# Performance work log

Hardware: AMD Instinct MI355X
Metric: run time of the kernel (lower is better)

Reference implementation:

```python
import jax, jax.numpy as jnp
import numpy as np

DIM = 128
P = (2, 2, 2)
D_STATE = 8
D_CONV = 4
EXPAND = 2
D_INNER = EXPAND * DIM
DT_RANK = (DIM + 15) // 16  # ceil(d_model/16) = 8
EPS = 1e-5


def setup_inputs() -> dict:
    key = jax.random.key(0)
    ks = jax.random.split(key, 8)
    B, C, Z, H, W = 2, DIM, 40, 40, 40
    s = lambda k, shape, scale: jax.random.normal(k, shape, jnp.float32) * scale
    return {
        "x": jax.random.normal(ks[0], (B, C, Z, H, W), jnp.float32),
        "norm_g": jnp.ones((C,), jnp.float32),
        "norm_b": jnp.zeros((C,), jnp.float32),
        "in_proj_w": s(ks[1], (2 * D_INNER, C), 0.02),
        "conv_w": s(ks[2], (D_INNER, D_CONV), 0.1),
        "conv_b": jnp.zeros((D_INNER,), jnp.float32),
        "x_proj_w": s(ks[3], (DT_RANK + 2 * D_STATE, D_INNER), 0.02),
        "dt_proj_w": s(ks[4], (D_INNER, DT_RANK), 0.1),
        # softplus^-1(0.01): small positive init for delta, as in mamba_ssm
        "dt_bias": jnp.log(jnp.expm1(jnp.full((D_INNER,), 0.01, jnp.float32))),
        # S4D-real init: A_log = log([1..d_state]) per channel
        "A_log": jnp.log(jnp.tile(jnp.arange(1, D_STATE + 1, dtype=jnp.float32), (D_INNER, 1))),
        "D_vec": jnp.ones((D_INNER,), jnp.float32),
        "out_proj_w": s(ks[5], (DIM, D_INNER), 0.02),
    }


def _mamba(xn, in_proj_w, conv_w, conv_b, x_proj_w, dt_proj_w, dt_bias, A_log, D_vec, out_proj_w):
    # xn: (NB, L, C)
    NB, L, _ = xn.shape
    xz = jnp.einsum('blc,ec->ble', xn, in_proj_w)          # (NB, L, 2*d_inner)
    xp, z = jnp.split(xz, 2, axis=-1)
    # causal depthwise conv1d, kernel D_CONV, truncated to L
    xpad = jnp.pad(xp, ((0, 0), (D_CONV - 1, 0), (0, 0)))
    conv = conv_b
    for k in range(D_CONV):
        conv = conv + xpad[:, k:k + L, :] * conv_w[:, k]
    u = jax.nn.silu(conv)                                  # (NB, L, d_inner)
    xdbl = jnp.einsum('bld,ed->ble', u, x_proj_w)
    dt, Bm, Cm = jnp.split(xdbl, [DT_RANK, DT_RANK + D_STATE], axis=-1)
    delta = jax.nn.softplus(jnp.einsum('blr,dr->bld', dt, dt_proj_w) + dt_bias)
    A = -jnp.exp(A_log)                                    # (d_inner, d_state)

    def step(h, inp):
        d_t, B_t, C_t, u_t = inp  # (NB,d_inner),(NB,d_state),(NB,d_state),(NB,d_inner)
        h = jnp.exp(d_t[:, :, None] * A) * h + (d_t * u_t)[:, :, None] * B_t[:, None, :]
        return h, jnp.einsum('bds,bs->bd', h, C_t)

    h0 = jnp.zeros((NB, D_INNER, D_STATE), xn.dtype)
    xs = (jnp.swapaxes(delta, 0, 1), jnp.swapaxes(Bm, 0, 1),
          jnp.swapaxes(Cm, 0, 1), jnp.swapaxes(u, 0, 1))
    _, ys = jax.lax.scan(step, h0, xs)                     # ys: (L, NB, d_inner)
    y = jnp.swapaxes(ys, 0, 1) + u * D_vec
    y = y * jax.nn.silu(z)
    return jnp.einsum('bld,cd->blc', y, out_proj_w)        # (NB, L, C)


def reference(x, norm_g, norm_b, in_proj_w, conv_w, conv_b, x_proj_w, dt_proj_w,
              dt_bias, A_log, D_vec, out_proj_w):
    B, C, Z, H, W = x.shape
    p1, p2, p3 = P
    NZ, NH, NW = Z // p1, H // p2, W // p3
    NB, L = B * p1 * p2 * p3, NZ * NH * NW
    # patch reshuffle: (B,C,Z,H,W) -> (B*p1*p2*p3, C, NZ, NH, NW)
    xd = x.reshape(B, C, NZ, p1, NH, p2, NW, p3).transpose(0, 3, 5, 7, 1, 2, 4, 6)
    xf = jnp.swapaxes(xd.reshape(NB, C, L), 1, 2)          # (NB, L, C)
    # LayerNorm over channel dim
    mu = xf.mean(-1, keepdims=True)
    var = xf.var(-1, keepdims=True)
    xn = (xf - mu) * jax.lax.rsqrt(var + EPS) * norm_g + norm_b
    yo = _mamba(xn, in_proj_w, conv_w, conv_b, x_proj_w, dt_proj_w, dt_bias,
                A_log, D_vec, out_proj_w)                  # (NB, L, C)
    # undo reshuffle
    xo = jnp.swapaxes(yo, 1, 2).reshape(B, p1, p2, p3, C, NZ, NH, NW)
    xo = xo.transpose(0, 4, 5, 1, 6, 2, 7, 3).reshape(B, C, Z, H, W)
    return xo + x
```

## Files before the change

kernel.cpp:

```cpp
#include <hip/hip_runtime.h>

#define NBATCH 16
#define LSEQ   8000
#define MROWS  128000
#define CDIM   128
#define DI     256
#define DS     8
#define DTR    8
#define NXP    24
#define NC     250
#define CL     32

#define OFF_PB    0ull
#define OFF_XN    1024000ull
#define OFF_STA   1024000ull
#define OFF_XP    33792000ull
#define OFF_XDBL  33792000ull
#define OFF_STH   46080000ull
#define OFF_ZS    99328000ull
#define OFF_U     164864000ull
#define WS_NEEDED 230400000ull

#define P_G    0
#define P_B    128
#define P_IPW  256
#define P_CW   65792
#define P_CB   66816
#define P_XPW  67072
#define P_DTW  73216
#define P_DTB  75264
#define P_ALOG 75520
#define P_DVEC 77568
#define P_OPW  77824
#define P_TOT  110592

typedef __attribute__((ext_vector_type(8))) short bf16x8;
typedef __attribute__((ext_vector_type(4))) float f32x4;
typedef __attribute__((ext_vector_type(2))) float f32x2;

__device__ __forceinline__ float bf2f(unsigned short a) {
    union { unsigned int u; float f; } v; v.u = ((unsigned int)a) << 16; return v.f;
}
__device__ __forceinline__ unsigned short f2bf(float f) {
    union { float f; unsigned int u; } v; v.f = f;
    unsigned int r = v.u + 0x7FFFu + ((v.u >> 16) & 1u);
    return (unsigned short)(r >> 16);
}
__device__ __forceinline__ unsigned short f2bf_cvt(float f) {
    unsigned int r;
    asm("v_cvt_pk_bf16_f32 %0, %1, %2" : "=v"(r) : "v"(f), "v"(0.f));
    return (unsigned short)r;
}
__device__ __forceinline__ bool bfmode(const void* g) {
    return ((const unsigned int*)g)[0] == 0x3F803F80u;
}
__device__ __forceinline__ float rd(const void* p, size_t i, bool bf) {
    return bf ? bf2f(((const unsigned short*)p)[i]) : ((const float*)p)[i];
}
__device__ __forceinline__ f32x2 pk_fma(f32x2 a, f32x2 b, f32x2 c) {
    f32x2 d;
    asm("v_pk_fma_f32 %0, %1, %2, %3" : "=v"(d) : "v"(a), "v"(b), "v"(c));
    return d;
}
__device__ __forceinline__ f32x2 pk_mul(f32x2 a, f32x2 b) {
    f32x2 d;
    asm("v_pk_mul_f32 %0, %1, %2" : "=v"(d) : "v"(a), "v"(b));
    return d;
}
__device__ __forceinline__ int m_of(int b, int sp) {
    int z = sp / 1600;
    int rem = sp - z * 1600;
    int h = rem / 40;
    int w = rem - h * 40;
    int nb = b * 8 + (z & 1) * 4 + (h & 1) * 2 + (w & 1);
    int l = (z >> 1) * 400 + (h >> 1) * 20 + (w >> 1);
    return nb * LSEQ + l;
}

__global__ __launch_bounds__(256) void param_convert(const void* g, const void* b, const void* ipw,
                                                     const void* cw, const void* cb, const void* xpw,
                                                     const void* dtw, const void* dtb, const void* alog,
                                                     const void* dvec, const void* opw,
                                                     unsigned short* __restrict__ pb)
{
    int gid = blockIdx.x * 256 + threadIdx.x;
    if (gid >= P_TOT) return;
    bool bf = bfmode(g);
    const void* src; int off;
    if      (gid < P_B)    { src = g;    off = P_G; }
    else if (gid < P_IPW)  { src = b;    off = P_B; }
    else if (gid < P_CW)   { src = ipw;  off = P_IPW; }
    else if (gid < P_CB)   { src = cw;   off = P_CW; }
    else if (gid < P_XPW)  { src = cb;   off = P_CB; }
    else if (gid < P_DTW)  { src = xpw;  off = P_XPW; }
    else if (gid < P_DTB)  { src = dtw;  off = P_DTW; }
    else if (gid < P_ALOG) { src = dtb;  off = P_DTB; }
    else if (gid < P_DVEC) { src = alog; off = P_ALOG; }
    else if (gid < P_OPW)  { src = dvec; off = P_DVEC; }
    else                   { src = opw;  off = P_OPW; }
    pb[gid] = f2bf(rd(src, gid - off, bf));
}

__global__ __launch_bounds__(256) void lnorm_kernel(const void* __restrict__ x,
                                                    const unsigned short* __restrict__ pb,
                                                    unsigned short* __restrict__ xn)
{
    __shared__ float tile[128][65];
    __shared__ float psum[4][64], psqs[4][64];
    __shared__ float smu[64], srs[64];
    int b  = blockIdx.y;
    int sp0 = blockIdx.x * 64;
    int t = threadIdx.x;

    int spi = t & 63, cpart = t >> 6;
    const float* xf = (const float*)x;
#pragma unroll
    for (int pass = 0; pass < 32; ++pass) {
        int c = pass * 4 + cpart;
        tile[c][spi] = xf[((size_t)b * CDIM + c) * 64000 + sp0 + spi];
    }
    __syncthreads();

    {
        float s = 0.f, ss = 0.f;
        int c0 = cpart * 32;
#pragma unroll
        for (int cc = 0; cc < 32; ++cc) {
            float v = tile[c0 + cc][spi];
            s += v; ss += v * v;
        }
        psum[cpart][spi] = s; psqs[cpart][spi] = ss;
    }
    __syncthreads();
    if (cpart == 0) {
        float s  = psum[0][spi] + psum[1][spi] + psum[2][spi] + psum[3][spi];
        float ss = psqs[0][spi] + psqs[1][spi] + psqs[2][spi] + psqs[3][spi];
        float m = s * (1.f / CDIM);
        float var = ss * (1.f / CDIM) - m * m;
        smu[spi] = m;
        srs[spi] = rsqrtf(var + 1e-5f);
    }
    __syncthreads();

    int c = t & 127, half = t >> 7;
    float gc = bf2f(pb[P_G + c]), bc = bf2f(pb[P_B + c]);
#pragma unroll
    for (int pass = 0; pass < 32; ++pass) {
        int j = pass * 2 + half;
        int m = m_of(b, sp0 + j);
        float v = (tile[c][j] - smu[j]) * srs[j] * gc + bc;
        xn[(size_t)m * CDIM + c] = f2bf(v);
    }
}

__global__ __launch_bounds__(256) void gemm_bt_kernel(const unsigned short* __restrict__ A,
                                                      const unsigned short* __restrict__ W,
                                                      void* __restrict__ D,
                                                      int K, int Nact, int ldd, int act)
{
    __shared__ unsigned short As[128 * 32];
    __shared__ unsigned short Ws[128 * 32];
    int tid = threadIdx.x;
    int m0 = blockIdx.x * 128;
    int n0 = blockIdx.y * 128;
    int wave = tid >> 6, lane = tid & 63;
    int wm = (wave & 1) * 64, wn = (wave >> 1) * 64;
    int lrow = lane & 15, lk = (lane >> 4) * 8;
    int quad = lane >> 4;

    f32x4 acc[4][4];
#pragma unroll
    for (int i = 0; i < 4; i++)
#pragma unroll
        for (int j = 0; j < 4; j++) acc[i][j] = (f32x4){0.f, 0.f, 0.f, 0.f};

    int rowA0 = tid >> 2, kcA0 = (tid & 3) << 3;
    int rowA1 = (tid + 256) >> 2, kcA1 = (tid & 3) << 3;

    for (int kt = 0; kt < K; kt += 32) {
        *(uint4*)&As[rowA0 * 32 + kcA0] = *(const uint4*)&A[(size_t)(m0 + rowA0) * K + kt + kcA0];
        *(uint4*)&As[rowA1 * 32 + kcA1] = *(const uint4*)&A[(size_t)(m0 + rowA1) * K + kt + kcA1];
        uint4 z4 = {0u, 0u, 0u, 0u};
        uint4 w0 = (n0 + rowA0 < Nact) ? *(const uint4*)&W[(size_t)(n0 + rowA0) * K + kt + kcA0] : z4;
        uint4 w1 = (n0 + rowA1 < Nact) ? *(const uint4*)&W[(size_t)(n0 + rowA1) * K + kt + kcA1] : z4;
        *(uint4*)&Ws[rowA0 * 32 + kcA0] = w0;
        *(uint4*)&Ws[rowA1 * 32 + kcA1] = w1;
        __syncthreads();

        bf16x8 af[4], bfr[4];
#pragma unroll
        for (int i = 0; i < 4; i++) af[i]  = *(const bf16x8*)&As[(wm + i * 16 + lrow) * 32 + lk];
#pragma unroll
        for (int j = 0; j < 4; j++) bfr[j] = *(const bf16x8*)&Ws[(wn + j * 16 + lrow) * 32 + lk];
#pragma unroll
        for (int i = 0; i < 4; i++)
#pragma unroll
            for (int j = 0; j < 4; j++)
                acc[i][j] = __builtin_amdgcn_mfma_f32_16x16x32_bf16(af[i], bfr[j], acc[i][j], 0, 0, 0);
        __syncthreads();
    }

#pragma unroll
    for (int i = 0; i < 4; i++)
#pragma unroll
        for (int j = 0; j < 4; j++) {
            int n = n0 + wn + j * 16 + lrow;
            if (n < Nact) {
#pragma unroll
                for (int r = 0; r < 4; r++) {
                    int m = m0 + wm + i * 16 + quad * 4 + r;
                    float v = acc[i][j][r];
                    if (act == 1) v = v / (1.f + __expf(-v));
                    ((unsigned short*)D)[(size_t)m * ldd + n] = f2bf(v);
                }
            }
        }
}

__global__ __launch_bounds__(256) void gemm_conv_kernel(const unsigned short* __restrict__ A,
                                                        const unsigned short* __restrict__ W,
                                                        const unsigned short* __restrict__ cw,
                                                        const unsigned short* __restrict__ cb,
                                                        unsigned short* __restrict__ u)
{
    __shared__ unsigned short As[128 * 32];
    __shared__ unsigned short Ws[128 * 32];
    __shared__ unsigned short Dt[128 * 132];

    int tid = threadIdx.x;
    int tile = blockIdx.x & 63;
    int nb = blockIdx.x >> 6;
    int n0 = blockIdx.y * 128;
    int m0 = nb * 8000 + tile * 125;
    int mA = m0 - 3;
    int wave = tid >> 6, lane = tid & 63;
    int wm = (wave & 1) * 64, wn = (wave >> 1) * 64;
    int lrow = lane & 15, lk = (lane >> 4) * 8;
    int quad = lane >> 4;

    f32x4 acc[4][4];
#pragma unroll
    for (int i = 0; i < 4; i++)
#pragma unroll
        for (int j = 0; j < 4; j++) acc[i][j] = (f32x4){0.f, 0.f, 0.f, 0.f};

    int rowA0 = tid >> 2, kcA0 = (tid & 3) << 3;
    int rowA1 = (tid + 256) >> 2;

    for (int kt = 0; kt < CDIM; kt += 32) {
        uint4 z4 = {0u, 0u, 0u, 0u};
        uint4 a0 = (tile == 0 && rowA0 < 3) ? z4
                 : *(const uint4*)&A[(size_t)(mA + rowA0) * CDIM + kt + kcA0];
        uint4 a1 = *(const uint4*)&A[(size_t)(mA + rowA1) * CDIM + kt + kcA0];
        *(uint4*)&As[rowA0 * 32 + kcA0] = a0;
        *(uint4*)&As[rowA1 * 32 + kcA0] = a1;
        *(uint4*)&Ws[rowA0 * 32 + kcA0] = *(const uint4*)&W[(size_t)(n0 + rowA0) * CDIM + kt + kcA0];
        *(uint4*)&Ws[rowA1 * 32 + kcA0] = *(const uint4*)&W[(size_t)(n0 + rowA1) * CDIM + kt + kcA0];
        __syncthreads();

        bf16x8 af[4], bfr[4];
#pragma unroll
        for (int i = 0; i < 4; i++) af[i]  = *(const bf16x8*)&As[(wm + i * 16 + lrow) * 32 + lk];
#pragma unroll
        for (int j = 0; j < 4; j++) bfr[j] = *(const bf16x8*)&Ws[(wn + j * 16 + lrow) * 32 + lk];
#pragma unroll
        for (int i = 0; i < 4; i++)
#pragma unroll
            for (int j = 0; j < 4; j++)
                acc[i][j] = __builtin_amdgcn_mfma_f32_16x16x32_bf16(af[i], bfr[j], acc[i][j], 0, 0, 0);
        __syncthreads();
    }

#pragma unroll
    for (int i = 0; i < 4; i++)
#pragma unroll
        for (int j = 0; j < 4; j++) {
            int nl = wn + j * 16 + lrow;
            int tr = wm + i * 16 + quad * 4;
            unsigned int c01, c23;
            asm("v_cvt_pk_bf16_f32 %0, %1, %2" : "=v"(c01) : "v"(acc[i][j][0]), "v"(acc[i][j][1]));
            asm("v_cvt_pk_bf16_f32 %0, %1, %2" : "=v"(c23) : "v"(acc[i][j][2]), "v"(acc[i][j][3]));
            *(unsigned int*)&Dt[nl * 132 + tr]     = c01;
            *(unsigned int*)&Dt[nl * 132 + tr + 2] = c23;
        }
    __syncthreads();

    {
        int nl = tid & 127, half = tid >> 7;
        int dch = n0 + nl;
        float cw0 = bf2f(cw[dch * 4 + 0]), cw1 = bf2f(cw[dch * 4 + 1]);
        float cw2 = bf2f(cw[dch * 4 + 2]), cw3 = bf2f(cw[dch * 4 + 3]);
        float cbv = bf2f(cb[dch]);
        int tr0 = half ? 66 : 3;
        int nsteps = half ? 62 : 63;
        const unsigned short* col = &Dt[nl * 132];
        float x0 = bf2f(col[tr0 - 3]), x1 = bf2f(col[tr0 - 2]), x2 = bf2f(col[tr0 - 1]);
        unsigned short* uout = &u[(size_t)(m0 + tr0 - 3) * DI + dch];
#pragma unroll 1
        for (int k = 0; k < nsteps; ++k) {
            float x3 = bf2f(col[tr0 + k]);
            float a = cbv + cw0 * x0 + cw1 * x1 + cw2 * x2 + cw3 * x3;
            float uv = a * __builtin_amdgcn_rcpf(1.f + __expf(-a));
            *uout = f2bf_cvt(uv);
            uout += DI;
            x0 = x1; x1 = x2; x2 = x3;
        }
    }
}


#define BODY1(UR, RO) do {                                                       \
    union { f32x4 q; f32x2 h[2]; } qa, qb, qc, qd;                               \
    qa.q = *(const f32x4*)(rfp + (RO));                                          \
    qb.q = *(const f32x4*)(rfp + (RO) + 4);                                      \
    qc.q = *(const f32x4*)(rfp + (RO) + 8);                                      \
    qd.q = *(const f32x4*)(rfp + (RO) + 12);                                     \
    f32x2 din2 = pk_fma(qa.h[0], Wq[0], bias2);                                  \
    din2 = pk_fma(qa.h[1], Wq[1], din2);                                         \
    din2 = pk_fma(qb.h[0], Wq[2], din2);                                         \
    din2 = pk_fma(qb.h[1], Wq[3], din2);                                         \
    float din = din2.x + din2.y;                                                 \
    float e = __expf(din);                                                       \
    float w = 1.f + e;                                                           \
    float p1 = __builtin_amdgcn_rcpf(w);                                         \
    float delta = (din > 15.f) ? din : __logf(w);                                \
    float du = delta * bf2f(UR);                                                 \
    float p2 = p1 * p1;                                                          \
    f32x2 q1; q1.x = p1; q1.y = p2;                                              \
    f32x2 pp2; pp2.x = p2; pp2.y = p2;                                           \
    f32x2 q2 = pk_mul(q1, pp2);                                                  \
    f32x2 pp4; pp4.x = q2.y; pp4.y = q2.y;                                       \
    f32x2 q3 = pk_mul(q1, pp4);                                                  \
    f32x2 q4 = pk_mul(q2, pp4);                                                  \
    f32x2 du2; du2.x = du; du2.y = du;                                           \
    h2[0] = pk_fma(du2, qc.h[0], pk_mul(q1, h2[0]));                             \
    h2[1] = pk_fma(du2, qc.h[1], pk_mul(q2, h2[1]));                             \
    h2[2] = pk_fma(du2, qd.h[0], pk_mul(q3, h2[2]));                             \
    h2[3] = pk_fma(du2, qd.h[1], pk_mul(q4, h2[3]));                             \
    P *= p1;                                                                     \
} while (0)

__global__ __launch_bounds__(256) void gemm_xdbl_scan1(const unsigned short* __restrict__ u,
                                                       const unsigned short* __restrict__ W,
                                                       const unsigned short* __restrict__ dtw,
                                                       const unsigned short* __restrict__ dtb,
                                                       const unsigned short* __restrict__ alog,
                                                       float* __restrict__ xdbl,
                                                       float* __restrict__ stA,
                                                       float* __restrict__ stH)
{
    __shared__ unsigned short As[64 * 32];
    __shared__ unsigned short Ws[32 * 32];
    __shared__ float Dxs[64 * NXP];
    int tid = threadIdx.x;
    int m0 = blockIdx.x * 64;
    int wave = tid >> 6, lane = tid & 63;
    int wm = (wave & 1) * 32, wn = (wave >> 1) * 16;
    int lrow = lane & 15, lk = (lane >> 4) * 8;
    int quad = lane >> 4;

    f32x4 acc[2];
    acc[0] = (f32x4){0.f, 0.f, 0.f, 0.f};
    acc[1] = (f32x4){0.f, 0.f, 0.f, 0.f};

    int rowA = tid >> 2, kcA = (tid & 3) << 3;

    for (int kt = 0; kt < DI; kt += 32) {
        *(uint4*)&As[rowA * 32 + kcA] = *(const uint4*)&u[(size_t)(m0 + rowA) * DI + kt + kcA];
        if (tid < 128) {
            uint4 z4 = {0u, 0u, 0u, 0u};
            int rw = tid >> 2;
            uint4 w0 = (rw < NXP) ? *(const uint4*)&W[(size_t)rw * DI + kt + kcA] : z4;
            *(uint4*)&Ws[rw * 32 + kcA] = w0;
        }
        __syncthreads();

        bf16x8 af0 = *(const bf16x8*)&As[(wm + lrow) * 32 + lk];
        bf16x8 af1 = *(const bf16x8*)&As[(wm + 16 + lrow) * 32 + lk];
        bf16x8 bfr = *(const bf16x8*)&Ws[(wn + lrow) * 32 + lk];
        acc[0] = __builtin_amdgcn_mfma_f32_16x16x32_bf16(af0, bfr, acc[0], 0, 0, 0);
        acc[1] = __builtin_amdgcn_mfma_f32_16x16x32_bf16(af1, bfr, acc[1], 0, 0, 0);
        __syncthreads();
    }

    {
        int n = wn + lrow;
        if (n < NXP) {
#pragma unroll
            for (int i = 0; i < 2; i++)
#pragma unroll
                for (int r = 0; r < 4; r++) {
                    int ml = wm + i * 16 + quad * 4 + r;
                    float v = acc[i][r];
                    xdbl[(size_t)(m0 + ml) * NXP + n] = v;
                    Dxs[ml * NXP + n] = v;
                }
        }
    }
    __syncthreads();

    int d = tid;
    f32x2 Wq[4];
#pragma unroll
    for (int r = 0; r < 4; r++) {
        Wq[r].x = bf2f(dtw[d * DTR + 2 * r]);
        Wq[r].y = bf2f(dtw[d * DTR + 2 * r + 1]);
    }
    float Av[DS];
#pragma unroll
    for (int s = 0; s < DS; s++) Av[s] = -__expf(bf2f(alog[d * DS + s]));
    float A1 = Av[0];
    bool fast = (A1 == -1.0f);
#pragma unroll
    for (int s = 1; s < DS; s++)
        fast = fast && (fabsf(Av[s] - (float)(s + 1) * A1) <= 0.02f * (float)(s + 1) * fabsf(A1));
    float bias = bf2f(dtb[d]);
    f32x2 bias2; bias2.x = bias; bias2.y = 0.f;

#pragma unroll 1
    for (int k = 0; k < 2; ++k) {
        int gm0 = m0 + 32 * k;
        int nb = gm0 / 8000;
        int cc = (gm0 - nb * 8000) >> 5;
        size_t o = (((size_t)cc * NBATCH + nb) * DI + d) * DS;
        const unsigned short* up = u + (size_t)gm0 * DI + d;
        const float* rfp = &Dxs[32 * k * NXP];

        if (fast) {
            f32x2 h2[4];
#pragma unroll
            for (int i = 0; i < 4; i++) { h2[i].x = 0.f; h2[i].y = 0.f; }
            float P = 1.f;
            unsigned short u0 = up[0], u1 = up[DI];
            const unsigned short* uld = up + 2 * DI;
#pragma unroll 1
            for (int t = 0; t < CL - 2; t += 2) {
                unsigned short ua = uld[0], ub = uld[DI]; uld += 2 * DI;
                BODY1(u0, 0);
                BODY1(u1, NXP);
                u0 = ua; u1 = ub;
                rfp += 2 * NXP;
            }
            BODY1(u0, 0);
            BODY1(u1, NXP);
            float P2 = P * P, P3 = P2 * P, P4 = P2 * P2;
            float apv[DS] = {P, P2, P3, P4, P4 * P, P3 * P3, P4 * P3, P4 * P4};
#pragma unroll
            for (int s = 0; s < DS; s++) stA[o + s] = apv[s];
#pragma unroll
            for (int i = 0; i < 4; i++) { stH[o + 2 * i] = h2[i].x; stH[o + 2 * i + 1] = h2[i].y; }
        } else {
            float Wdt[DTR];
#pragma unroll
            for (int r = 0; r < 4; r++) { Wdt[2 * r] = Wq[r].x; Wdt[2 * r + 1] = Wq[r].y; }
            float h[DS], ap[DS];
#pragma unroll
            for (int s = 0; s < DS; s++) { h[s] = 0.f; ap[s] = 1.f; }
            const unsigned short* uld = up;
#pragma unroll 1
            for (int t = 0; t < CL; ++t) {
                float uv = bf2f(*uld); uld += DI;
                float din = bias;
#pragma unroll
                for (int r = 0; r < DTR; r++) din += rfp[r] * Wdt[r];
                float delta = (din > 15.f) ? din : __logf(1.f + __expf(din));
                float du = delta * uv;
#pragma unroll
                for (int s = 0; s < DS; s++) {
                    float dA = __expf(delta * Av[s]);
                    h[s] = dA * h[s] + du * rfp[8 + s];
                    ap[s] *= dA;
                }
                rfp += NXP;
            }
#pragma unroll
            for (int s = 0; s < DS; s++) { stA[o + s] = ap[s]; stH[o + s] = h[s]; }
        }
    }
}

__global__ __launch_bounds__(256) void scan_phase2(float* __restrict__ stA, float* __restrict__ stH)
{
    size_t t = blockIdx.x * 256 + threadIdx.x;
    const size_t stride = (size_t)NBATCH * DI * DS;
    float hin = 0.f;
    size_t idx = t;
    float a[10], hl[10], an[10], hn[10];
#pragma unroll
    for (int j = 0; j < 10; ++j) { a[j] = stA[idx + j * stride]; hl[j] = stH[idx + j * stride]; }
#pragma unroll 1
    for (int g = 0; g < 25; ++g) {
        size_t nidx = idx + 10 * stride;
        if (g < 24) {
#pragma unroll
            for (int j = 0; j < 10; ++j) { an[j] = stA[nidx + j * stride]; hn[j] = stH[nidx + j * stride]; }
        }
#pragma unroll
        for (int j = 0; j < 10; ++j) {
            stH[idx + j * stride] = hin;
            hin = a[j] * hin + hl[j];
        }
#pragma unroll
        for (int j = 0; j < 10; ++j) { a[j] = an[j]; hl[j] = hn[j]; }
        idx = nidx;
    }
}

#define BODY3Y(UR, ZR, RO, T) do {                                               \
    union { f32x4 q; f32x2 h[2]; } qa, qb, qc, qd, qe, qf;                       \
    qa.q = *(const f32x4*)(rfp + (RO));                                          \
    qb.q = *(const f32x4*)(rfp + (RO) + 4);                                      \
    qc.q = *(const f32x4*)(rfp + (RO) + 8);                                      \
    qd.q = *(const f32x4*)(rfp + (RO) + 12);                                     \
    qe.q = *(const f32x4*)(rfp + (RO) + 16);                                     \
    qf.q = *(const f32x4*)(rfp + (RO) + 20);                                     \
    f32x2 din2 = pk_fma(qa.h[0], Wq[0], bias2);                                  \
    din2 = pk_fma(qa.h[1], Wq[1], din2);                                         \
    din2 = pk_fma(qb.h[0], Wq[2], din2);                                         \
    din2 = pk_fma(qb.h[1], Wq[3], din2);                                         \
    float din = din2.x + din2.y;                                                 \
    float e = __expf(din);                                                       \
    float w = 1.f + e;                                                           \
    float p1 = __builtin_amdgcn_rcpf(w);                                         \
    float delta = (din > 15.f) ? din : __logf(w);                                \
    float uv = bf2f(UR);                                                         \
    float du = delta * uv;                                                       \
    float p2 = p1 * p1;                                                          \
    f32x2 q1; q1.x = p1; q1.y = p2;                                              \
    f32x2 pp2; pp2.x = p2; pp2.y = p2;                                           \
    f32x2 q2 = pk_mul(q1, pp2);                                                  \
    f32x2 pp4; pp4.x = q2.y; pp4.y = q2.y;                                       \
    f32x2 q3 = pk_mul(q1, pp4);                                                  \
    f32x2 q4 = pk_mul(q2, pp4);                                                  \
    f32x2 du2; du2.x = du; du2.y = du;                                           \
    h2[0] = pk_fma(du2, qc.h[0], pk_mul(q1, h2[0]));                             \
    h2[1] = pk_fma(du2, qc.h[1], pk_mul(q2, h2[1]));                             \
    h2[2] = pk_fma(du2, qd.h[0], pk_mul(q3, h2[2]));                             \
    h2[3] = pk_fma(du2, qd.h[1], pk_mul(q4, h2[3]));                             \
    f32x2 y2v = pk_mul(h2[0], qe.h[0]);                                          \
    y2v = pk_fma(h2[1], qe.h[1], y2v);                                           \
    y2v = pk_fma(h2[2], qf.h[0], y2v);                                           \
    y2v = pk_fma(h2[3], qf.h[1], y2v);                                           \
    float y = __builtin_fmaf(uv, Dv, y2v.x) + y2v.y;                             \
    ytcol[(T) * 264] = f2bf_cvt(y * bf2f(ZR));                                   \
} while (0)

__global__ __launch_bounds__(256) void scan3_gemm_out(const unsigned short* __restrict__ zs,
                                                      const unsigned short* __restrict__ u,
                                                      const float* __restrict__ xdbl,
                                                      const unsigned short* __restrict__ dtw,
                                                      const unsigned short* __restrict__ dtb,
                                                      const unsigned short* __restrict__ alog,
                                                      const unsigned short* __restrict__ dvec,
                                                      const float* __restrict__ stH,
                                                      const unsigned short* __restrict__ W,
                                                      unsigned short* __restrict__ y2)
{
    __shared__ float xs[CL * NXP];
    __shared__ unsigned short Yt[CL * 264];
    int tid = threadIdx.x;
    int gm0 = blockIdx.x * 32;
    int nb = gm0 / 8000;
    int c  = (gm0 - nb * 8000) >> 5;
    int d = tid;
    size_t base = (size_t)gm0;
    {
        const uint4* src = (const uint4*)(xdbl + base * NXP);
        uint4* dst = (uint4*)xs;
        if (tid < 192) dst[tid] = src[tid];
    }
    f32x2 Wq[4];
#pragma unroll
    for (int r = 0; r < 4; r++) {
        Wq[r].x = bf2f(dtw[d * DTR + 2 * r]);
        Wq[r].y = bf2f(dtw[d * DTR + 2 * r + 1]);
    }
    float Av[DS];
#pragma unroll
    for (int s = 0; s < DS; s++) Av[s] = -__expf(bf2f(alog[d * DS + s]));
    float A1 = Av[0];
    bool fast = (A1 == -1.0f);
#pragma unroll
    for (int s = 1; s < DS; s++)
        fast = fast && (fabsf(Av[s] - (float)(s + 1) * A1) <= 0.02f * (float)(s + 1) * fabsf(A1));
    float bias = bf2f(dtb[d]);
    f32x2 bias2; bias2.x = bias; bias2.y = 0.f;
    float Dv = bf2f(dvec[d]);
    size_t o = (((size_t)c * NBATCH + nb) * DI + d) * DS;
    const unsigned short* up = u + base * DI + d;
    const unsigned short* zp = zs + base * DI + d;
    unsigned short* ytcol = &Yt[d];
    __syncthreads();

    if (fast) {
        f32x2 h2[4];
#pragma unroll
        for (int i = 0; i < 4; i++) { h2[i].x = stH[o + 2 * i]; h2[i].y = stH[o + 2 * i + 1]; }
        const float* rfp = xs;
        unsigned short u0 = up[0], u1 = up[DI];
        unsigned short z0 = zp[0], z1 = zp[DI];
        const unsigned short* uld = up + 2 * DI;
        const unsigned short* zld = zp + 2 * DI;
#pragma unroll 1
        for (int t = 0; t < CL - 2; t += 2) {
            unsigned short ua = uld[0], ub = uld[DI]; uld += 2 * DI;
            unsigned short za = zld[0], zb = zld[DI]; zld += 2 * DI;
            BODY3Y(u0, z0, 0, t);
            BODY3Y(u1, z1, NXP, t + 1);
            u0 = ua; u1 = ub; z0 = za; z1 = zb;
            rfp += 2 * NXP;
        }
        BODY3Y(u0, z0, 0, CL - 2);
        BODY3Y(u1, z1, NXP, CL - 1);
    } else {
        float Wdt[DTR];
#pragma unroll
        for (int r = 0; r < 4; r++) { Wdt[2 * r] = Wq[r].x; Wdt[2 * r + 1] = Wq[r].y; }
        float h[DS];
#pragma unroll
        for (int s = 0; s < DS; s++) h[s] = stH[o + s];
        const float* rfp = xs;
        const unsigned short* uld = up;
        const unsigned short* zld = zp;
#pragma unroll 1
        for (int t = 0; t < CL; ++t) {
            float uv = bf2f(*uld); uld += DI;
            float szv = bf2f(*zld); zld += DI;
            float din = bias;
#pragma unroll
            for (int r = 0; r < DTR; r++) din += rfp[r] * Wdt[r];
            float delta = (din > 15.f) ? din : __logf(1.f + __expf(din));
            float du = delta * uv;
            float y = 0.f;
#pragma unroll
            for (int s = 0; s < DS; s++) {
                float dA = __expf(delta * Av[s]);
                h[s] = dA * h[s] + du * rfp[8 + s];
                y += h[s] * rfp[16 + s];
            }
            y += uv * Dv;
            ytcol[t * 264] = f2bf_cvt(y * szv);
            rfp += NXP;
        }
    }
    __syncthreads();

    {
        int wave = tid >> 6, lane = tid & 63;
        int wn = wave * 32;
        int lrow = lane & 15, lk = (lane >> 4) * 8;
        int quad = lane >> 4;
        f32x4 acc[2][2];
#pragma unroll
        for (int i = 0; i < 2; i++)
#pragma unroll
            for (int j = 0; j < 2; j++) acc[i][j] = (f32x4){0.f, 0.f, 0.f, 0.f};

        for (int kt = 0; kt < DI; kt += 32) {
            bf16x8 af[2], bfr[2];
#pragma unroll
            for (int i = 0; i < 2; i++)
                af[i] = *(const bf16x8*)&Yt[(i * 16 + lrow) * 264 + kt + lk];
#pragma unroll
            for (int j = 0; j < 2; j++)
                bfr[j] = *(const bf16x8*)&W[(size_t)(wn + j * 16 + lrow) * DI + kt + lk];
#pragma unroll
            for (int i = 0; i < 2; i++)
#pragma unroll
                for (int j = 0; j < 2; j++)
                    acc[i][j] = __builtin_amdgcn_mfma_f32_16x16x32_bf16(af[i], bfr[j], acc[i][j], 0, 0, 0);
        }

#pragma unroll
        for (int i = 0; i < 2; i++)
#pragma unroll
            for (int j = 0; j < 2; j++) {
                int n = wn + j * 16 + lrow;
#pragma unroll
                for (int r = 0; r < 4; r++) {
                    int m = i * 16 + quad * 4 + r;
                    y2[(size_t)(gm0 + m) * CDIM + n] = f2bf_cvt(acc[i][j][r]);
                }
            }
    }
}

__global__ __launch_bounds__(256) void unpatch_kernel(const void* __restrict__ x,
                                                      const unsigned short* __restrict__ y2,
                                                      float* __restrict__ out)
{
    __shared__ float ytile[64][129];
    int b  = blockIdx.y;
    int sp0 = blockIdx.x * 64;
    int t = threadIdx.x;

    {
        int c = t & 127, half = t >> 7;
#pragma unroll
        for (int pass = 0; pass < 32; ++pass) {
            int j = pass * 2 + half;
            int m = m_of(b, sp0 + j);
            ytile[j][c] = bf2f(y2[(size_t)m * CDIM + c]);
        }
    }
    __syncthreads();

    const float* xf = (const float*)x;
    int spi = t & 63, cpart = t >> 6;
#pragma unroll
    for (int pass = 0; pass < 32; ++pass) {
        int c = pass * 4 + cpart;
        size_t idx = ((size_t)b * CDIM + c) * 64000 + sp0 + spi;
        out[idx] = xf[idx] + ytile[spi][c];
    }
}

extern "C" void kernel_launch(void* const* d_in, const int* in_sizes, int n_in,
                              void* d_out, int out_size, void* d_ws, size_t ws_size,
                              hipStream_t stream)
{
    const void* x     = d_in[0];
    const void* ng    = d_in[1];
    const void* nb_   = d_in[2];
    const void* ipw   = d_in[3];
    const void* cw    = d_in[4];
    const void* cb    = d_in[5];
    const void* xpw   = d_in[6];
    const void* dtw   = d_in[7];
    const void* dtb   = d_in[8];
    const void* alog  = d_in[9];
    const void* dvec  = d_in[10];
    const void* opw   = d_in[11];
    float* out = (float*)d_out;

    if (ws_size < WS_NEEDED) return;

    char* ws = (char*)d_ws;
    unsigned short* pb   = (unsigned short*)(ws + OFF_PB);
    unsigned short* xn   = (unsigned short*)(ws + OFF_XN);
    float* stA = (float*)(ws + OFF_STA);
    float* stH = (float*)(ws + OFF_STH);
    float* xdblf = (float*)(ws + OFF_XDBL);
    unsigned short* zs   = (unsigned short*)(ws + OFF_ZS);
    unsigned short* u    = (unsigned short*)(ws + OFF_U);
    unsigned short* y2   = xn;

    param_convert<<<432, 256, 0, stream>>>(ng, nb_, ipw, cw, cb, xpw, dtw, dtb, alog, dvec, opw, pb);
    lnorm_kernel<<<dim3(1000, 2), 256, 0, stream>>>(x, pb, xn);
    gemm_conv_kernel<<<dim3(1024, 2), 256, 0, stream>>>(xn, pb + P_IPW, pb + P_CW, pb + P_CB, u);
    gemm_bt_kernel<<<dim3(1000, 2), 256, 0, stream>>>(xn, pb + P_IPW + 256 * 128, zs, CDIM, DI, DI, 1);
    gemm_xdbl_scan1<<<2000, 256, 0, stream>>>(u, pb + P_XPW, pb + P_DTW, pb + P_DTB,
                                              pb + P_ALOG, xdblf, stA, stH);
    scan_phase2<<<128, 256, 0, stream>>>(stA, stH);
    scan3_gemm_out<<<4000, 256, 0, stream>>>(zs, u, xdblf, pb + P_DTW, pb + P_DTB,
                                             pb + P_ALOG, pb + P_DVEC, stH, pb + P_OPW, y2);
    unpatch_kernel<<<dim3(1000, 2), 256, 0, stream>>>(x, y2, out);
}
```

Baseline: 373.9 us.

## Fuse z-projection GEMM and SiLU gate into scan3 output kernel

Drops the standalone gemm_bt_kernel that wrote silu(z) to global memory. The scan3 kernel now computes the z half of in_proj per 32-row tile with MFMA from xn staged in shared memory, applies SiLU, and stores the result in a shared buffer that is later overwritten in place with y*silu(z) for the out projection. This removes the 65 MB zs write and read plus one launch, at the cost of extra shared memory, registers and barriers in scan3. It also requires xn to stay valid until scan3, so stA is relocated into the freed zs region.

Result: faster. 364.6 us (-2.5%).

```diff
diff --git a/kernel.cpp b/kernel.cpp
--- a/kernel.cpp
+++ b/kernel.cpp
@@ -13,11 +13,10 @@
 
 #define OFF_PB    0ull
 #define OFF_XN    1024000ull
-#define OFF_STA   1024000ull
 #define OFF_XP    33792000ull
 #define OFF_XDBL  33792000ull
 #define OFF_STH   46080000ull
-#define OFF_ZS    99328000ull
+#define OFF_STA   99328000ull
 #define OFF_U     164864000ull
 #define WS_NEEDED 230400000ull
 
@@ -151,70 +150,6 @@
         float v = (tile[c][j] - smu[j]) * srs[j] * gc + bc;
         xn[(size_t)m * CDIM + c] = f2bf(v);
     }
-}
-
-__global__ __launch_bounds__(256) void gemm_bt_kernel(const unsigned short* __restrict__ A,
-                                                      const unsigned short* __restrict__ W,
-                                                      void* __restrict__ D,
-                                                      int K, int Nact, int ldd, int act)
-{
-    __shared__ unsigned short As[128 * 32];
-    __shared__ unsigned short Ws[128 * 32];
-    int tid = threadIdx.x;
-    int m0 = blockIdx.x * 128;
-    int n0 = blockIdx.y * 128;
-    int wave = tid >> 6, lane = tid & 63;
-    int wm = (wave & 1) * 64, wn = (wave >> 1) * 64;
-    int lrow = lane & 15, lk = (lane >> 4) * 8;
-    int quad = lane >> 4;
-
-    f32x4 acc[4][4];
-#pragma unroll
-    for (int i = 0; i < 4; i++)
-#pragma unroll
-        for (int j = 0; j < 4; j++) acc[i][j] = (f32x4){0.f, 0.f, 0.f, 0.f};
-
-    int rowA0 = tid >> 2, kcA0 = (tid & 3) << 3;
-    int rowA1 = (tid + 256) >> 2, kcA1 = (tid & 3) << 3;
-
-    for (int kt = 0; kt < K; kt += 32) {
-        *(uint4*)&As[rowA0 * 32 + kcA0] = *(const uint4*)&A[(size_t)(m0 + rowA0) * K + kt + kcA0];
-        *(uint4*)&As[rowA1 * 32 + kcA1] = *(const uint4*)&A[(size_t)(m0 + rowA1) * K + kt + kcA1];
-        uint4 z4 = {0u, 0u, 0u, 0u};
-        uint4 w0 = (n0 + rowA0 < Nact) ? *(const uint4*)&W[(size_t)(n0 + rowA0) * K + kt + kcA0] : z4;
-        uint4 w1 = (n0 + rowA1 < Nact) ? *(const uint4*)&W[(size_t)(n0 + rowA1) * K + kt + kcA1] : z4;
-        *(uint4*)&Ws[rowA0 * 32 + kcA0] = w0;
-        *(uint4*)&Ws[rowA1 * 32 + kcA1] = w1;
-        __syncthreads();
-
-        bf16x8 af[4], bfr[4];
-#pragma unroll
-        for (int i = 0; i < 4; i++) af[i]  = *(const bf16x8*)&As[(wm + i * 16 + lrow) * 32 + lk];
-#pragma unroll
-        for (int j = 0; j < 4; j++) bfr[j] = *(const bf16x8*)&Ws[(wn + j * 16 + lrow) * 32 + lk];
-#pragma unroll
-        for (int i = 0; i < 4; i++)
-#pragma unroll
-            for (int j = 0; j < 4; j++)
-                acc[i][j] = __builtin_amdgcn_mfma_f32_16x16x32_bf16(af[i], bfr[j], acc[i][j], 0, 0, 0);
-        __syncthreads();
-    }
-
-#pragma unroll
-    for (int i = 0; i < 4; i++)
-#pragma unroll
-        for (int j = 0; j < 4; j++) {
-            int n = n0 + wn + j * 16 + lrow;
-            if (n < Nact) {
-#pragma unroll
-                for (int r = 0; r < 4; r++) {
-                    int m = m0 + wm + i * 16 + quad * 4 + r;
-                    float v = acc[i][j][r];
-                    if (act == 1) v = v / (1.f + __expf(-v));
-                    ((unsigned short*)D)[(size_t)m * ldd + n] = f2bf(v);
-                }
-            }
-        }
 }
 
 __global__ __launch_bounds__(256) void gemm_conv_kernel(const unsigned short* __restrict__ A,
@@ -506,7 +441,7 @@
     }
 }
 
-#define BODY3Y(UR, ZR, RO, T) do {                                               \
+#define BODY3Z(UR, RO, T) do {                                                   \
     union { f32x4 q; f32x2 h[2]; } qa, qb, qc, qd, qe, qf;                       \
     qa.q = *(const f32x4*)(rfp + (RO));                                          \
     qb.q = *(const f32x4*)(rfp + (RO) + 4);                                      \
@@ -542,10 +477,11 @@
     y2v = pk_fma(h2[2], qf.h[0], y2v);                                           \
     y2v = pk_fma(h2[3], qf.h[1], y2v);                                           \
     float y = __builtin_fmaf(uv, Dv, y2v.x) + y2v.y;                             \
-    ytcol[(T) * 264] = f2bf_cvt(y * bf2f(ZR));                                   \
+    float szv = bf2f(zycol[(T) * 264]);                                          \
+    zycol[(T) * 264] = f2bf_cvt(y * szv);                                        \
 } while (0)
 
-__global__ __launch_bounds__(256) void scan3_gemm_out(const unsigned short* __restrict__ zs,
+__global__ __launch_bounds__(256) void scan3_gemm_out(const unsigned short* __restrict__ xn,
                                                       const unsigned short* __restrict__ u,
                                                       const float* __restrict__ xdbl,
                                                       const unsigned short* __restrict__ dtw,
@@ -553,22 +489,75 @@
                                                       const unsigned short* __restrict__ alog,
                                                       const unsigned short* __restrict__ dvec,
                                                       const float* __restrict__ stH,
-                                                      const unsigned short* __restrict__ W,
+                                                      const unsigned short* __restrict__ Wz,
+                                                      const unsigned short* __restrict__ Wo,
                                                       unsigned short* __restrict__ y2)
 {
+    union Sh3 { unsigned short As[32 * 136]; unsigned short ZY[CL * 264]; };
     __shared__ float xs[CL * NXP];
-    __shared__ unsigned short Yt[CL * 264];
+    __shared__ Sh3 sh;
     int tid = threadIdx.x;
     int gm0 = blockIdx.x * 32;
     int nb = gm0 / 8000;
     int c  = (gm0 - nb * 8000) >> 5;
     int d = tid;
     size_t base = (size_t)gm0;
+    int wave = tid >> 6, lane = tid & 63;
+    int lrow = lane & 15, lk = (lane >> 4) * 8;
+    int quad = lane >> 4;
+
     {
         const uint4* src = (const uint4*)(xdbl + base * NXP);
         uint4* dst = (uint4*)xs;
         if (tid < 192) dst[tid] = src[tid];
-    }
+        int rr = tid >> 3, qq = tid & 7;
+        const uint4* xsrc = (const uint4*)&xn[(size_t)(gm0 + rr) * CDIM];
+        uint4* dstA = (uint4*)&sh.As[rr * 136];
+        dstA[qq] = xsrc[qq];
+        dstA[qq + 8] = xsrc[qq + 8];
+    }
+    __syncthreads();
+
+    {
+        int wnz = wave * 64;
+        f32x4 zacc[2][4];
+#pragma unroll
+        for (int i = 0; i < 2; i++)
+#pragma unroll
+            for (int j = 0; j < 4; j++) zacc[i][j] = (f32x4){0.f, 0.f, 0.f, 0.f};
+
+        for (int kt = 0; kt < CDIM; kt += 32) {
+            bf16x8 af[2], bfr[4];
+#pragma unroll
+            for (int i = 0; i < 2; i++)
+                af[i] = *(const bf16x8*)&sh.As[(i * 16 + lrow) * 136 + kt + lk];
+#pragma unroll
+            for (int j = 0; j < 4; j++)
+                bfr[j] = *(const bf16x8*)&Wz[(size_t)(wnz + j * 16 + lrow) * CDIM + kt + lk];
+#pragma unroll
+            for (int i = 0; i < 2; i++)
+#pragma unroll
+                for (int j = 0; j < 4; j++)
+                    zacc[i][j] = __builtin_amdgcn_mfma_f32_16x16x32_bf16(af[i], bfr[j], zacc[i][j], 0, 0, 0);
+        }
+        __syncthreads();
+
+#pragma unroll
+        for (int i = 0; i < 2; i++)
+#pragma unroll
+            for (int j = 0; j < 4; j++) {
+                int dch = wnz + j * 16 + lrow;
+#pragma unroll
+                for (int r = 0; r < 4; r++) {
+                    int m = i * 16 + quad * 4 + r;
+                    float v = zacc[i][j][r];
+                    float sz = v * __builtin_amdgcn_rcpf(1.f + __expf(-v));
+                    sh.ZY[m * 264 + dch] = f2bf_cvt(sz);
+                }
+            }
+    }
+    __syncthreads();
+
     f32x2 Wq[4];
 #pragma unroll
     for (int r = 0; r < 4; r++) {
@@ -588,9 +577,7 @@
     float Dv = bf2f(dvec[d]);
     size_t o = (((size_t)c * NBATCH + nb) * DI + d) * DS;
     const unsigned short* up = u + base * DI + d;
-    const unsigned short* zp = zs + base * DI + d;
-    unsigned short* ytcol = &Yt[d];
-    __syncthreads();
+    unsigned short* zycol = &sh.ZY[d];
 
     if (fast) {
         f32x2 h2[4];
@@ -598,20 +585,17 @@
         for (int i = 0; i < 4; i++) { h2[i].x = stH[o + 2 * i]; h2[i].y = stH[o + 2 * i + 1]; }
         const float* rfp = xs;
         unsigned short u0 = up[0], u1 = up[DI];
-        unsigned short z0 = zp[0], z1 = zp[DI];
         const unsigned short* uld = up + 2 * DI;
-        const unsigned short* zld = zp + 2 * DI;
 #pragma unroll 1
         for (int t = 0; t < CL - 2; t += 2) {
             unsigned short ua = uld[0], ub = uld[DI]; uld += 2 * DI;
-            unsigned short za = zld[0], zb = zld[DI]; zld += 2 * DI;
-            BODY3Y(u0, z0, 0, t);
-            BODY3Y(u1, z1, NXP, t + 1);
-            u0 = ua; u1 = ub; z0 = za; z1 = zb;
+            BODY3Z(u0, 0, t);
+            BODY3Z(u1, NXP, t + 1);
+            u0 = ua; u1 = ub;
             rfp += 2 * NXP;
         }
-        BODY3Y(u0, z0, 0, CL - 2);
-        BODY3Y(u1, z1, NXP, CL - 1);
+        BODY3Z(u0, 0, CL - 2);
+        BODY3Z(u1, NXP, CL - 1);
     } else {
         float Wdt[DTR];
 #pragma unroll
@@ -621,11 +605,10 @@
         for (int s = 0; s < DS; s++) h[s] = stH[o + s];
         const float* rfp = xs;
         const unsigned short* uld = up;
-        const unsigned short* zld = zp;
 #pragma unroll 1
         for (int t = 0; t < CL; ++t) {
             float uv = bf2f(*uld); uld += DI;
-            float szv = bf2f(*zld); zld += DI;
+            float szv = bf2f(zycol[t * 264]);
             float din = bias;
 #pragma unroll
             for (int r = 0; r < DTR; r++) din += rfp[r] * Wdt[r];
@@ -639,17 +622,14 @@
                 y += h[s] * rfp[16 + s];
             }
             y += uv * Dv;
-            ytcol[t * 264] = f2bf_cvt(y * szv);
+            zycol[t * 264] = f2bf_cvt(y * szv);
             rfp += NXP;
         }
     }
     __syncthreads();
 
     {
-        int wave = tid >> 6, lane = tid & 63;
         int wn = wave * 32;
-        int lrow = lane & 15, lk = (lane >> 4) * 8;
-        int quad = lane >> 4;
         f32x4 acc[2][2];
 #pragma unroll
         for (int i = 0; i < 2; i++)
@@ -660,10 +640,10 @@
             bf16x8 af[2], bfr[2];
 #pragma unroll
             for (int i = 0; i < 2; i++)
-                af[i] = *(const bf16x8*)&Yt[(i * 16 + lrow) * 264 + kt + lk];
+                af[i] = *(const bf16x8*)&sh.ZY[(i * 16 + lrow) * 264 + kt + lk];
 #pragma unroll
             for (int j = 0; j < 2; j++)
-                bfr[j] = *(const bf16x8*)&W[(size_t)(wn + j * 16 + lrow) * DI + kt + lk];
+                bfr[j] = *(const bf16x8*)&Wo[(size_t)(wn + j * 16 + lrow) * DI + kt + lk];
 #pragma unroll
             for (int i = 0; i < 2; i++)
 #pragma unroll
@@ -741,18 +721,17 @@
     float* stA = (float*)(ws + OFF_STA);
     float* stH = (float*)(ws + OFF_STH);
     float* xdblf = (float*)(ws + OFF_XDBL);
-    unsigned short* zs   = (unsigned short*)(ws + OFF_ZS);
     unsigned short* u    = (unsigned short*)(ws + OFF_U);
     unsigned short* y2   = xn;
 
     param_convert<<<432, 256, 0, stream>>>(ng, nb_, ipw, cw, cb, xpw, dtw, dtb, alog, dvec, opw, pb);
     lnorm_kernel<<<dim3(1000, 2), 256, 0, stream>>>(x, pb, xn);
     gemm_conv_kernel<<<dim3(1024, 2), 256, 0, stream>>>(xn, pb + P_IPW, pb + P_CW, pb + P_CB, u);
-    gemm_bt_kernel<<<dim3(1000, 2), 256, 0, stream>>>(xn, pb + P_IPW + 256 * 128, zs, CDIM, DI, DI, 1);
     gemm_xdbl_scan1<<<2000, 256, 0, stream>>>(u, pb + P_XPW, pb + P_DTW, pb + P_DTB,
                                               pb + P_ALOG, xdblf, stA, stH);
     scan_phase2<<<128, 256, 0, stream>>>(stA, stH);
-    scan3_gemm_out<<<4000, 256, 0, stream>>>(zs, u, xdblf, pb + P_DTW, pb + P_DTB,
-                                             pb + P_ALOG, pb + P_DVEC, stH, pb + P_OPW, y2);
+    scan3_gemm_out<<<4000, 256, 0, stream>>>(xn, u, xdblf, pb + P_DTW, pb + P_DTB,
+                                             pb + P_ALOG, pb + P_DVEC, stH,
+                                             pb + P_IPW + 256 * 128, pb + P_OPW, y2);
     unpatch_kernel<<<dim3(1000, 2), 256, 0, stream>>>(x, y2, out);
 }
```
